# Performance work log

Hardware: AMD Instinct MI355X
Metric: run time of the kernel (lower is better)

Reference implementation:

```python
import jax, jax.numpy as jnp
import numpy as np

B, N, D_IN, D_OUT = 16, 2048, 128, 128

def setup_inputs() -> dict:
    key = jax.random.key(0)
    ks = jax.random.split(key, 8)
    x = jax.random.normal(ks[0], (B, N, D_IN), dtype=jnp.float32)
    adj = jax.random.randint(ks[1], (N, N), 0, 2).astype(jnp.float32)
    # Conv1d(kernel_size=1) weights, PyTorch default uniform init scale
    s_emb = 1.0 / np.sqrt(D_IN)
    W_emb = jax.random.uniform(ks[2], (D_OUT, D_IN), jnp.float32, -s_emb, s_emb)
    b_emb = jax.random.uniform(ks[3], (D_OUT,), jnp.float32, -s_emb, s_emb)
    s_qk = 1.0 / np.sqrt(D_OUT)
    w_q = jax.random.uniform(ks[4], (D_OUT,), jnp.float32, -s_qk, s_qk)
    b_q = jax.random.uniform(ks[5], (1,), jnp.float32, -s_qk, s_qk)
    w_k = jax.random.uniform(ks[6], (D_OUT,), jnp.float32, -s_qk, s_qk)
    b_k = jax.random.uniform(ks[7], (1,), jnp.float32, -s_qk, s_qk)
    return {"x": x, "adj": adj, "W_emb": W_emb, "b_emb": b_emb,
            "w_q": w_q, "b_q": b_q, "w_k": w_k, "b_k": b_k}

def reference(x, adj, W_emb, b_emb, w_q, b_q, w_k, b_k):
    # emb_conv: 1x1 conv over node dim == per-node linear  [B,N,D_out]
    seq_fts = jnp.einsum('bni,oi->bno', x, W_emb) + b_emb
    # q_conv / k_conv: project to scalar per node  [B,N]
    q = jnp.einsum('bnd,d->bn', seq_fts, w_q) + b_q  # f_1_t squeezed
    k = jnp.einsum('bnd,d->bn', seq_fts, w_k) + b_k  # f_2_t squeezed
    # f[b,i,j] = f_1_t[b,0,j] + f_2_t^T[b,i,0] = q[b,j] + k[b,i]
    f = k[:, :, None] + q[:, None, :]                 # [B,N,N]
    f = jax.nn.leaky_relu(adj[None, :, :] * f, negative_slope=0.01)
    coefs = jax.nn.softmax(f, axis=1)                 # softmax over dim=1 (rows)
    vals = jnp.einsum('bij,bjd->bid', coefs, seq_fts)  # [B,N,D_out]
    return vals
```

## Files before the change

### kernel.cpp

```cpp
#include <hip/hip_runtime.h>
#include <hip/hip_bf16.h>
#include <stdint.h>

#define B_ 16
#define N_ 2048
#define D_ 128

typedef __bf16 bf16_t;
typedef bf16_t bf16x8 __attribute__((ext_vector_type(8)));
typedef float f32x4 __attribute__((ext_vector_type(4)));

__global__ __launch_bounds__(256) void k_pack_adj(const float* __restrict__ adj,
                                                  unsigned int* __restrict__ bits) {
    int t = blockIdx.x * 256 + threadIdx.x;
    float v = adj[t];
    unsigned long long m = __ballot(v > 0.5f);
    if ((t & 63) == 0) {
        int i = t >> 11;
        int j = t & 2047;
        bits[i * 64 + (j >> 5)]     = (unsigned int)m;
        bits[i * 64 + (j >> 5) + 1] = (unsigned int)(m >> 32);
    }
}

__global__ __launch_bounds__(256, 2) void k_emb(const float* __restrict__ x,
                                                const float* __restrict__ W,
                                                const float* __restrict__ be,
                                                const float* __restrict__ wq,
                                                const float* __restrict__ bq,
                                                const float* __restrict__ wk,
                                                const float* __restrict__ bk,
                                                float* __restrict__ sfT,
                                                float* __restrict__ qa, float* __restrict__ ka,
                                                float* __restrict__ Eq, float* __restrict__ eqs,
                                                float* __restrict__ Ek, float* __restrict__ eks) {
    __shared__ float xs[32][68];
    __shared__ float ws[32][132];
    __shared__ float qs[64], ks[64];
    int b  = blockIdx.y;
    int n0 = blockIdx.x * 64;
    int tid = threadIdx.x;
    int tx = tid & 15, ty = tid >> 4;
    if (tid < 64) { qs[tid] = 0.f; ks[tid] = 0.f; }

    float acc[4][8] = {};
    f32x4 xr[2], wr[4];

    auto loadregs = [&](int kc) {
#pragma unroll
        for (int s = 0; s < 2; ++s) {
            int p = tid + 256 * s;
            int n = p >> 3, kq = p & 7;
            xr[s] = *(const f32x4*)(x + ((size_t)(b * N_ + n0 + n)) * D_ + kc * 32 + kq * 4);
        }
#pragma unroll
        for (int s = 0; s < 4; ++s) {
            int p = tid + 256 * s;
            int d = p >> 3, kq = p & 7;
            wr[s] = *(const f32x4*)(W + (size_t)d * D_ + kc * 32 + kq * 4);
        }
    };
    auto writelds = [&]() {
#pragma unroll
        for (int s = 0; s < 2; ++s) {
            int p = tid + 256 * s;
            int n = p >> 3, kq = p & 7;
#pragma unroll
            for (int u = 0; u < 4; ++u) xs[kq * 4 + u][n] = xr[s][u];
        }
#pragma unroll
        for (int s = 0; s < 4; ++s) {
            int p = tid + 256 * s;
            int d = p >> 3, kq = p & 7;
#pragma unroll
            for (int u = 0; u < 4; ++u) ws[kq * 4 + u][d] = wr[s][u];
        }
    };

    loadregs(0);
    for (int kc = 0; kc < 4; ++kc) {
        writelds();
        __syncthreads();
        if (kc < 3) loadregs(kc + 1);
#pragma unroll 4
        for (int k = 0; k < 32; ++k) {
            f32x4 xv  = *(const f32x4*)&xs[k][tx * 4];
            f32x4 wv0 = *(const f32x4*)&ws[k][ty * 8];
            f32x4 wv1 = *(const f32x4*)&ws[k][ty * 8 + 4];
#pragma unroll
            for (int i = 0; i < 4; ++i)
#pragma unroll
                for (int j = 0; j < 8; ++j)
                    acc[i][j] += xv[i] * ((j < 4) ? wv0[j] : wv1[j - 4]);
        }
        __syncthreads();
    }

    float qp[4] = {}, kp[4] = {};
#pragma unroll
    for (int j = 0; j < 8; ++j) {
        int d = ty * 8 + j;
        float bj  = be[d];
        float wqj = wq[d];
        float wkj = wk[d];
        f32x4 o;
#pragma unroll
        for (int i = 0; i < 4; ++i) {
            o[i] = acc[i][j] + bj;
            qp[i] += o[i] * wqj;
            kp[i] += o[i] * wkj;
        }
        *(f32x4*)(sfT + ((size_t)b * D_ + d) * N_ + n0 + tx * 4) = o;
    }
#pragma unroll
    for (int i = 0; i < 4; ++i) {
        atomicAdd(&qs[tx * 4 + i], qp[i]);
        atomicAdd(&ks[tx * 4 + i], kp[i]);
    }
    __syncthreads();
    if (tid < 64) {
        int idx = b * N_ + n0 + tid;
        float aq = qs[tid] + bq[0];
        float ak = ks[tid] + bk[0];
        qa[idx] = aq;          ka[idx] = ak;
        Eq[idx] = expf(aq);    eqs[idx] = expf(0.01f * aq);
        Ek[idx] = expf(ak);    eks[idx] = expf(0.01f * ak);
    }
}

__global__ __launch_bounds__(256) void k_denom(const unsigned int* __restrict__ bits,
                                               const float* __restrict__ qa,
                                               const float* __restrict__ ka,
                                               const float* __restrict__ Eq,
                                               const float* __restrict__ eqs,
                                               const float* __restrict__ Ek,
                                               const float* __restrict__ eks,
                                               float* __restrict__ denom) {
    int jt  = blockIdx.x;
    int b   = blockIdx.y;
    int seg = blockIdx.z;
    int j = jt * 256 + threadIdx.x;
    float qj  = qa[b * N_ + j];
    float Eqj = Eq[b * N_ + j];
    float eqj = eqs[b * N_ + j];
    int shift = j & 31;
    int wid   = j >> 5;
    float acc = 0.f;
    int i0 = seg * 256;
#pragma unroll 16
    for (int i = i0; i < i0 + 256; ++i) {
        float kk  = ka[b * N_ + i];
        float Ekk = Ek[b * N_ + i];
        float ekk = eks[b * N_ + i];
        unsigned int w = bits[i * 64 + wid];
        float z  = kk + qj;
        float f1 = z > 0.f ? Ekk : ekk;
        float f2 = z > 0.f ? Eqj : eqj;
        float v  = f1 * f2;
        acc += ((w >> shift) & 1u) ? v : 1.0f;
    }
    atomicAdd(&denom[b * N_ + j], acc);
}

__global__ __launch_bounds__(256) void k_scale(const float* __restrict__ sfT,
                                               const float* __restrict__ denom,
                                               bf16_t* __restrict__ Pt) {
    size_t t4 = ((size_t)blockIdx.x * 256 + threadIdx.x) * 4;
    int j  = (int)(t4 & (N_ - 1));
    int b  = (int)(t4 >> 18);
    f32x4 sv = *(const f32x4*)(sfT + t4);
    f32x4 dv = *(const f32x4*)(denom + b * N_ + j);
    bf16_t o[4];
#pragma unroll
    for (int u = 0; u < 4; ++u)
        o[u] = (bf16_t)(sv[u] * __builtin_amdgcn_rcpf(dv[u]));
    *(uint2*)(Pt + t4) = *(uint2*)o;
}

__global__ __launch_bounds__(256, 2) void k_attn(const float* __restrict__ qa,
                                                 const float* __restrict__ ka,
                                                 const float* __restrict__ Eq,
                                                 const float* __restrict__ eqs,
                                                 const float* __restrict__ Ek,
                                                 const float* __restrict__ eks,
                                                 const unsigned int* __restrict__ bits,
                                                 const bf16_t* __restrict__ Pt,
                                                 float* __restrict__ out) {
    __shared__ __align__(16) bf16_t ldsB[2][128 * 64];
    __shared__ __align__(16) bf16_t ldsA[4 * 2 * 64 * 8];
    int b     = blockIdx.y;
    int ibase = blockIdx.x * 64;
    int tid   = threadIdx.x;
    int w     = tid >> 6;
    int lane  = tid & 63;
    int m16   = lane & 15;
    int quad  = lane >> 4;
    int ig    = w & 1;
    int dg    = w >> 1;
    int h     = dg;

    int iA = ibase + (2 * ig) * 16 + m16;
    int iB = iA + 16;
    float kR0  = ka[b * N_ + iA],  kR1  = ka[b * N_ + iB];
    float EkR0 = Ek[b * N_ + iA],  EkR1 = Ek[b * N_ + iB];
    float ekR0 = eks[b * N_ + iA], ekR1 = eks[b * N_ + iB];
    const unsigned int* brA = bits + (size_t)iA * 64;
    const unsigned int* brB = bits + (size_t)iB * 64;
    const float* qp  = qa  + b * N_;
    const float* Eqp = Eq  + b * N_;
    const float* eqp = eqs + b * N_;
    const bf16_t* PtB = Pt + (size_t)b * D_ * N_;

    f32x4 acc[2][4];
#pragma unroll
    for (int c = 0; c < 2; ++c)
#pragma unroll
        for (int nt = 0; nt < 4; ++nt) acc[c][nt] = (f32x4){0.f, 0.f, 0.f, 0.f};

    auto stage = [&](int bufi, int jb) {
#pragma unroll
        for (int t = 0; t < 4; ++t) {
            int off = t * 4096 + tid * 16;
            int d   = off >> 7;
            int g   = ((off & 127) >> 4) ^ (d & 7);
            const bf16_t* gp = PtB + (size_t)d * N_ + jb + g * 8;
            __builtin_amdgcn_global_load_lds(
                (const __attribute__((address_space(1))) void*)gp,
                (__attribute__((address_space(3))) void*)((char*)(&ldsB[bufi][0]) + off),
                16, 0, 0);
        }
    };

    stage(0, 0);
    __syncthreads();
    int buf = 0;
    for (int step = 0; step < N_ / 64; ++step) {
        int jb = step * 64;

        int j0 = jb + h * 32 + quad * 8;
        f32x4 q0 = *(const f32x4*)(qp  + j0);
        f32x4 q1 = *(const f32x4*)(qp  + j0 + 4);
        f32x4 E0 = *(const f32x4*)(Eqp + j0);
        f32x4 E1 = *(const f32x4*)(Eqp + j0 + 4);
        f32x4 e0 = *(const f32x4*)(eqp + j0);
        f32x4 e1 = *(const f32x4*)(eqp + j0 + 4);
        unsigned int wA = brA[(jb >> 5) + h];
        unsigned int wB = brB[(jb >> 5) + h];
        __builtin_amdgcn_sched_barrier(0);

        if (step + 1 < N_ / 64) stage(buf ^ 1, jb + 64);

        bf16x8 afA, afB;
#pragma unroll
        for (int t = 0; t < 8; ++t) {
            float qv = (t < 4) ? q0[t] : q1[t - 4];
            float Ev = (t < 4) ? E0[t] : E1[t - 4];
            float ev = (t < 4) ? e0[t] : e1[t - 4];
            int bit = quad * 8 + t;
            {
                float z = kR0 + qv;
                float v = ((z > 0.f) ? EkR0 : ekR0) * ((z > 0.f) ? Ev : ev);
                afA[t] = (bf16_t)(((wA >> bit) & 1u) ? v : 1.0f);
            }
            {
                float z = kR1 + qv;
                float v = ((z > 0.f) ? EkR1 : ekR1) * ((z > 0.f) ? Ev : ev);
                afB[t] = (bf16_t)(((wB >> bit) & 1u) ? v : 1.0f);
            }
        }
        *(bf16x8*)((char*)ldsA + ((((2 * ig + 0) * 2 + h) * 64 + lane) * 16)) = afA;
        *(bf16x8*)((char*)ldsA + ((((2 * ig + 1) * 2 + h) * 64 + lane) * 16)) = afB;

        asm volatile("s_waitcnt lgkmcnt(0)\n\ts_barrier" ::: "memory");

#pragma unroll
        for (int hh = 0; hh < 2; ++hh) {
            bf16x8 a0 = *(const bf16x8*)((char*)ldsA + ((((2 * ig + 0) * 2 + hh) * 64 + lane) * 16));
            bf16x8 a1 = *(const bf16x8*)((char*)ldsA + ((((2 * ig + 1) * 2 + hh) * 64 + lane) * 16));
            int cph = ((hh * 4 + quad) ^ (m16 & 7)) * 8;
#pragma unroll
            for (int nt = 0; nt < 4; ++nt) {
                int d = dg * 64 + nt * 16 + m16;
                bf16x8 bf = *(const bf16x8*)&ldsB[buf][d * 64 + cph];
                acc[0][nt] = __builtin_amdgcn_mfma_f32_16x16x32_bf16(a0, bf, acc[0][nt], 0, 0, 0);
                acc[1][nt] = __builtin_amdgcn_mfma_f32_16x16x32_bf16(a1, bf, acc[1][nt], 0, 0, 0);
            }
        }
        __syncthreads();
        buf ^= 1;
    }

#pragma unroll
    for (int c = 0; c < 2; ++c) {
        int irow = ibase + (2 * ig + c) * 16 + quad * 4;
#pragma unroll
        for (int nt = 0; nt < 4; ++nt) {
            int d = dg * 64 + nt * 16 + m16;
#pragma unroll
            for (int r = 0; r < 4; ++r)
                out[((size_t)b * N_ + irow + r) * D_ + d] = acc[c][nt][r];
        }
    }
}

extern "C" void kernel_launch(void* const* d_in, const int* in_sizes, int n_in,
                              void* d_out, int out_size, void* d_ws, size_t ws_size,
                              hipStream_t stream) {
    const float* x   = (const float*)d_in[0];
    const float* adj = (const float*)d_in[1];
    const float* W   = (const float*)d_in[2];
    const float* be  = (const float*)d_in[3];
    const float* wq  = (const float*)d_in[4];
    const float* bq  = (const float*)d_in[5];
    const float* wk  = (const float*)d_in[6];
    const float* bk  = (const float*)d_in[7];
    float* out = (float*)d_out;

    char* ws = (char*)d_ws;
    size_t off = 0;
    float* sfT = (float*)(ws + off);  off += (size_t)B_ * D_ * N_ * 4;
    bf16_t* Pt = (bf16_t*)(ws + off); off += (size_t)B_ * D_ * N_ * 2;
    float* qa  = (float*)(ws + off);  off += (size_t)B_ * N_ * 4;
    float* ka  = (float*)(ws + off);  off += (size_t)B_ * N_ * 4;
    float* denom = (float*)(ws + off); off += (size_t)B_ * N_ * 4;
    float* Eq  = (float*)(ws + off);  off += (size_t)B_ * N_ * 4;
    float* eqs = (float*)(ws + off);  off += (size_t)B_ * N_ * 4;
    float* Ek  = (float*)(ws + off);  off += (size_t)B_ * N_ * 4;
    float* eks = (float*)(ws + off);  off += (size_t)B_ * N_ * 4;
    unsigned int* bits = (unsigned int*)(ws + off); off += (size_t)N_ * 64 * 4;

    hipMemsetAsync(denom, 0, (size_t)B_ * N_ * 4, stream);

    k_pack_adj<<<N_ * N_ / 256, 256, 0, stream>>>(adj, bits);
    k_emb<<<dim3(N_ / 64, B_), 256, 0, stream>>>(x, W, be, wq, bq, wk, bk,
                                                 sfT, qa, ka, Eq, eqs, Ek, eks);
    k_denom<<<dim3(8, 16, 8), 256, 0, stream>>>(bits, qa, ka, Eq, eqs, Ek, eks, denom);
    k_scale<<<B_ * D_ * N_ / 1024, 256, 0, stream>>>(sfT, denom, Pt);
    k_attn<<<dim3(N_ / 64, B_), 256, 0, stream>>>(qa, ka, Eq, eqs, Ek, eks, bits, Pt, out);
}
```

Before: 204.3 us.

## Fold softmax denominator into attention coefficients and drop scale kernel

k_emb now writes the embedding directly as bf16, and the separate k_scale pass is removed. The column-softmax denominator is applied inside k_attn by multiplying each coefficient by its reciprocal, and the z>0 test is rewritten as Eq_j > 1/Ek_i so the ka/qa loads go away. Each wave now builds its full A fragments in registers instead of sharing halves through LDS, which removes an LDS round trip and barrier per step at the cost of duplicated exp-product work. Per-column data is also prefetched one step ahead. Rounding the embedding to bf16 before the denominator scale changes rounding slightly, and the exp-comparison test can differ from z>0 near zero or under overflow.

After: 208.3 us. About the same (+2.0%).

```diff
diff --git a/kernel.cpp b/kernel.cpp
--- a/kernel.cpp
+++ b/kernel.cpp
@@ -30,7 +30,7 @@
                                                 const float* __restrict__ bq,
                                                 const float* __restrict__ wk,
                                                 const float* __restrict__ bk,
-                                                float* __restrict__ sfT,
+                                                bf16_t* __restrict__ Pb,
                                                 float* __restrict__ qa, float* __restrict__ ka,
                                                 float* __restrict__ Eq, float* __restrict__ eqs,
                                                 float* __restrict__ Ek, float* __restrict__ eks) {
@@ -104,13 +104,15 @@
         float wqj = wq[d];
         float wkj = wk[d];
         f32x4 o;
+        bf16_t ob[4];
 #pragma unroll
         for (int i = 0; i < 4; ++i) {
             o[i] = acc[i][j] + bj;
             qp[i] += o[i] * wqj;
             kp[i] += o[i] * wkj;
-        }
-        *(f32x4*)(sfT + ((size_t)b * D_ + d) * N_ + n0 + tx * 4) = o;
+            ob[i] = (bf16_t)o[i];
+        }
+        *(uint2*)(Pb + ((size_t)b * D_ + d) * N_ + n0 + tx * 4) = *(uint2*)ob;
     }
 #pragma unroll
     for (int i = 0; i < 4; ++i) {
@@ -162,32 +164,15 @@
     atomicAdd(&denom[b * N_ + j], acc);
 }
 
-__global__ __launch_bounds__(256) void k_scale(const float* __restrict__ sfT,
-                                               const float* __restrict__ denom,
-                                               bf16_t* __restrict__ Pt) {
-    size_t t4 = ((size_t)blockIdx.x * 256 + threadIdx.x) * 4;
-    int j  = (int)(t4 & (N_ - 1));
-    int b  = (int)(t4 >> 18);
-    f32x4 sv = *(const f32x4*)(sfT + t4);
-    f32x4 dv = *(const f32x4*)(denom + b * N_ + j);
-    bf16_t o[4];
-#pragma unroll
-    for (int u = 0; u < 4; ++u)
-        o[u] = (bf16_t)(sv[u] * __builtin_amdgcn_rcpf(dv[u]));
-    *(uint2*)(Pt + t4) = *(uint2*)o;
-}
-
-__global__ __launch_bounds__(256, 2) void k_attn(const float* __restrict__ qa,
-                                                 const float* __restrict__ ka,
-                                                 const float* __restrict__ Eq,
+__global__ __launch_bounds__(256, 2) void k_attn(const float* __restrict__ Eq,
                                                  const float* __restrict__ eqs,
                                                  const float* __restrict__ Ek,
                                                  const float* __restrict__ eks,
+                                                 const float* __restrict__ denom,
                                                  const unsigned int* __restrict__ bits,
-                                                 const bf16_t* __restrict__ Pt,
+                                                 const bf16_t* __restrict__ Pb,
                                                  float* __restrict__ out) {
     __shared__ __align__(16) bf16_t ldsB[2][128 * 64];
-    __shared__ __align__(16) bf16_t ldsA[4 * 2 * 64 * 8];
     int b     = blockIdx.y;
     int ibase = blockIdx.x * 64;
     int tid   = threadIdx.x;
@@ -197,25 +182,43 @@
     int quad  = lane >> 4;
     int ig    = w & 1;
     int dg    = w >> 1;
-    int h     = dg;
 
     int iA = ibase + (2 * ig) * 16 + m16;
     int iB = iA + 16;
-    float kR0  = ka[b * N_ + iA],  kR1  = ka[b * N_ + iB];
     float EkR0 = Ek[b * N_ + iA],  EkR1 = Ek[b * N_ + iB];
     float ekR0 = eks[b * N_ + iA], ekR1 = eks[b * N_ + iB];
+    float TR0 = __builtin_amdgcn_rcpf(EkR0);
+    float TR1 = __builtin_amdgcn_rcpf(EkR1);
     const unsigned int* brA = bits + (size_t)iA * 64;
     const unsigned int* brB = bits + (size_t)iB * 64;
-    const float* qp  = qa  + b * N_;
-    const float* Eqp = Eq  + b * N_;
-    const float* eqp = eqs + b * N_;
-    const bf16_t* PtB = Pt + (size_t)b * D_ * N_;
+    const float* Eqp = Eq    + b * N_;
+    const float* eqp = eqs   + b * N_;
+    const float* dnp = denom + b * N_;
+    const bf16_t* PtB = Pb + (size_t)b * D_ * N_;
 
     f32x4 acc[2][4];
 #pragma unroll
     for (int c = 0; c < 2; ++c)
 #pragma unroll
         for (int nt = 0; nt < 4; ++nt) acc[c][nt] = (f32x4){0.f, 0.f, 0.f, 0.f};
+
+    f32x4 Ev[2][2][2], ev[2][2][2], dv[2][2][2];
+    uint2 mA[2], mB[2];
+
+    auto ldj = [&](int par, int jb) {
+#pragma unroll
+        for (int hh = 0; hh < 2; ++hh) {
+            int j0 = jb + hh * 32 + quad * 8;
+            Ev[par][hh][0] = *(const f32x4*)(Eqp + j0);
+            Ev[par][hh][1] = *(const f32x4*)(Eqp + j0 + 4);
+            ev[par][hh][0] = *(const f32x4*)(eqp + j0);
+            ev[par][hh][1] = *(const f32x4*)(eqp + j0 + 4);
+            dv[par][hh][0] = *(const f32x4*)(dnp + j0);
+            dv[par][hh][1] = *(const f32x4*)(dnp + j0 + 4);
+        }
+        mA[par] = *(const uint2*)&brA[jb >> 5];
+        mB[par] = *(const uint2*)&brB[jb >> 5];
+    };
 
     auto stage = [&](int bufi, int jb) {
 #pragma unroll
@@ -232,62 +235,59 @@
     };
 
     stage(0, 0);
+    ldj(0, 0);
     __syncthreads();
     int buf = 0;
-    for (int step = 0; step < N_ / 64; ++step) {
-        int jb = step * 64;
-
-        int j0 = jb + h * 32 + quad * 8;
-        f32x4 q0 = *(const f32x4*)(qp  + j0);
-        f32x4 q1 = *(const f32x4*)(qp  + j0 + 4);
-        f32x4 E0 = *(const f32x4*)(Eqp + j0);
-        f32x4 E1 = *(const f32x4*)(Eqp + j0 + 4);
-        f32x4 e0 = *(const f32x4*)(eqp + j0);
-        f32x4 e1 = *(const f32x4*)(eqp + j0 + 4);
-        unsigned int wA = brA[(jb >> 5) + h];
-        unsigned int wB = brB[(jb >> 5) + h];
-        __builtin_amdgcn_sched_barrier(0);
-
-        if (step + 1 < N_ / 64) stage(buf ^ 1, jb + 64);
-
-        bf16x8 afA, afB;
-#pragma unroll
-        for (int t = 0; t < 8; ++t) {
-            float qv = (t < 4) ? q0[t] : q1[t - 4];
-            float Ev = (t < 4) ? E0[t] : E1[t - 4];
-            float ev = (t < 4) ? e0[t] : e1[t - 4];
-            int bit = quad * 8 + t;
-            {
-                float z = kR0 + qv;
-                float v = ((z > 0.f) ? EkR0 : ekR0) * ((z > 0.f) ? Ev : ev);
-                afA[t] = (bf16_t)(((wA >> bit) & 1u) ? v : 1.0f);
+#pragma unroll 1
+    for (int s2 = 0; s2 < N_ / 128; ++s2) {
+#pragma unroll
+        for (int par = 0; par < 2; ++par) {
+            int step = s2 * 2 + par;
+            int jb = step * 64;
+            if (step + 1 < N_ / 64) {
+                stage(buf ^ 1, jb + 64);
+                ldj(par ^ 1, jb + 64);
             }
-            {
-                float z = kR1 + qv;
-                float v = ((z > 0.f) ? EkR1 : ekR1) * ((z > 0.f) ? Ev : ev);
-                afB[t] = (bf16_t)(((wB >> bit) & 1u) ? v : 1.0f);
+
+            bf16x8 af[2][2];
+#pragma unroll
+            for (int hh = 0; hh < 2; ++hh) {
+                unsigned int wdA = hh ? mA[par].y : mA[par].x;
+                unsigned int wdB = hh ? mB[par].y : mB[par].x;
+#pragma unroll
+                for (int t = 0; t < 8; ++t) {
+                    float Eqj = (t < 4) ? Ev[par][hh][0][t] : Ev[par][hh][1][t - 4];
+                    float eqj = (t < 4) ? ev[par][hh][0][t] : ev[par][hh][1][t - 4];
+                    float dj  = (t < 4) ? dv[par][hh][0][t] : dv[par][hh][1][t - 4];
+                    float rdj = __builtin_amdgcn_rcpf(dj);
+                    int bit = quad * 8 + t;
+                    {
+                        bool c = Eqj > TR0;
+                        float v = (c ? EkR0 : ekR0) * (c ? Eqj : eqj) * rdj;
+                        af[0][hh][t] = (bf16_t)(((wdA >> bit) & 1u) ? v : rdj);
+                    }
+                    {
+                        bool c = Eqj > TR1;
+                        float v = (c ? EkR1 : ekR1) * (c ? Eqj : eqj) * rdj;
+                        af[1][hh][t] = (bf16_t)(((wdB >> bit) & 1u) ? v : rdj);
+                    }
+                }
             }
-        }
-        *(bf16x8*)((char*)ldsA + ((((2 * ig + 0) * 2 + h) * 64 + lane) * 16)) = afA;
-        *(bf16x8*)((char*)ldsA + ((((2 * ig + 1) * 2 + h) * 64 + lane) * 16)) = afB;
-
-        asm volatile("s_waitcnt lgkmcnt(0)\n\ts_barrier" ::: "memory");
-
-#pragma unroll
-        for (int hh = 0; hh < 2; ++hh) {
-            bf16x8 a0 = *(const bf16x8*)((char*)ldsA + ((((2 * ig + 0) * 2 + hh) * 64 + lane) * 16));
-            bf16x8 a1 = *(const bf16x8*)((char*)ldsA + ((((2 * ig + 1) * 2 + hh) * 64 + lane) * 16));
-            int cph = ((hh * 4 + quad) ^ (m16 & 7)) * 8;
-#pragma unroll
-            for (int nt = 0; nt < 4; ++nt) {
-                int d = dg * 64 + nt * 16 + m16;
-                bf16x8 bf = *(const bf16x8*)&ldsB[buf][d * 64 + cph];
-                acc[0][nt] = __builtin_amdgcn_mfma_f32_16x16x32_bf16(a0, bf, acc[0][nt], 0, 0, 0);
-                acc[1][nt] = __builtin_amdgcn_mfma_f32_16x16x32_bf16(a1, bf, acc[1][nt], 0, 0, 0);
+
+#pragma unroll
+            for (int hh = 0; hh < 2; ++hh) {
+                int cph = ((hh * 4 + quad) ^ (m16 & 7)) * 8;
+#pragma unroll
+                for (int nt = 0; nt < 4; ++nt) {
+                    int d = dg * 64 + nt * 16 + m16;
+                    bf16x8 bf = *(const bf16x8*)&ldsB[buf][d * 64 + cph];
+                    acc[0][nt] = __builtin_amdgcn_mfma_f32_16x16x32_bf16(af[0][hh], bf, acc[0][nt], 0, 0, 0);
+                    acc[1][nt] = __builtin_amdgcn_mfma_f32_16x16x32_bf16(af[1][hh], bf, acc[1][nt], 0, 0, 0);
+                }
             }
-        }
-        __syncthreads();
-        buf ^= 1;
+            __syncthreads();
+            buf ^= 1;
+        }
     }
 
 #pragma unroll
@@ -318,8 +318,7 @@
 
     char* ws = (char*)d_ws;
     size_t off = 0;
-    float* sfT = (float*)(ws + off);  off += (size_t)B_ * D_ * N_ * 4;
-    bf16_t* Pt = (bf16_t*)(ws + off); off += (size_t)B_ * D_ * N_ * 2;
+    bf16_t* Pb = (bf16_t*)(ws + off); off += (size_t)B_ * D_ * N_ * 2;
     float* qa  = (float*)(ws + off);  off += (size_t)B_ * N_ * 4;
     float* ka  = (float*)(ws + off);  off += (size_t)B_ * N_ * 4;
     float* denom = (float*)(ws + off); off += (size_t)B_ * N_ * 4;
@@ -333,8 +332,7 @@
 
     k_pack_adj<<<N_ * N_ / 256, 256, 0, stream>>>(adj, bits);
     k_emb<<<dim3(N_ / 64, B_), 256, 0, stream>>>(x, W, be, wq, bq, wk, bk,
-                                                 sfT, qa, ka, Eq, eqs, Ek, eks);
+                                                 Pb, qa, ka, Eq, eqs, Ek, eks);
     k_denom<<<dim3(8, 16, 8), 256, 0, stream>>>(bits, qa, ka, Eq, eqs, Ek, eks, denom);
-    k_scale<<<B_ * D_ * N_ / 1024, 256, 0, stream>>>(sfT, denom, Pt);
-    k_attn<<<dim3(N_ / 64, B_), 256, 0, stream>>>(qa, ka, Eq, eqs, Ek, eks, bits, Pt, out);
-}
+    k_attn<<<dim3(N_ / 64, B_), 256, 0, stream>>>(Eq, eqs, Ek, eks, denom, bits, Pb, out);
+}
```
